# Optimization experiments

Measured on AMD Instinct MI355X. Metric: run time of the kernel, lower is better.

Reference implementation:

```python
import jax, jax.numpy as jnp
import numpy as np

N_NODES = 100_000
N_EDGES = 1_600_000
N_GRAPHS = 512
NF = 64        # n_node_feats
H1 = 128       # hidden width
H2 = 64        # dim_node_emb
DIM_OUT = 1
STEPS = 4      # set2set processing steps


def _lin(x, W, b):
    # torch Linear convention: y = x @ W.T + b, W: [out, in]
    return x @ W.T + b


def _gelu(x):
    return jax.nn.gelu(x, approximate=False)  # torch.nn.GELU default (erf)


def _lstm_cell(x, h, c, Wih, Whh, bih, bhh):
    g = x @ Wih.T + bih + h @ Whh.T + bhh
    i, f, gg, o = jnp.split(g, 4, axis=-1)  # torch gate order: i, f, g, o
    i, f, o = jax.nn.sigmoid(i), jax.nn.sigmoid(f), jax.nn.sigmoid(o)
    gg = jnp.tanh(gg)
    c = f * c + i * gg
    h = o * jnp.tanh(c)
    return h, c


def setup_inputs() -> dict:
    key = jax.random.key(0)
    ks = jax.random.split(key, 24)
    p = lambda k, shp: jax.random.normal(k, shp, dtype=jnp.float32) * 0.05
    inp = {
        "x": jax.random.normal(ks[0], (N_NODES, NF), dtype=jnp.float32),
        "edge_index": jax.random.randint(ks[1], (2, N_EDGES), 0, N_NODES, dtype=jnp.int32),
        "batch": jnp.sort(jax.random.randint(ks[2], (N_NODES,), 0, N_GRAPHS, dtype=jnp.int32)),
        "nfc_W": p(ks[3], (H1, NF)), "nfc_b": p(ks[4], (H1,)),
        "gc1_W": p(ks[5], (H1, H1)), "gc1_b": p(ks[6], (H1,)),
        "gc2_W": p(ks[7], (H2, H1)), "gc2_b": p(ks[8], (H2,)),
        "lstm0_Wih": p(ks[9], (4 * H2, 2 * H2)), "lstm0_Whh": p(ks[10], (4 * H2, H2)),
        "lstm0_bih": p(ks[11], (4 * H2,)), "lstm0_bhh": p(ks[12], (4 * H2,)),
        "lstm1_Wih": p(ks[13], (4 * H2, H2)), "lstm1_Whh": p(ks[14], (4 * H2, H2)),
        "lstm1_bih": p(ks[15], (4 * H2,)), "lstm1_bhh": p(ks[16], (4 * H2,)),
        "fc1_W": p(ks[17], (32, 2 * H2)), "fc1_b": p(ks[18], (32,)),
        "fc2_W": p(ks[19], (DIM_OUT, 32)), "fc2_b": p(ks[20], (DIM_OUT,)),
    }
    return inp


def _forward(x, edge_index, batch, nfc_W, nfc_b, gc1_W, gc1_b, gc2_W, gc2_b,
             lstm0_Wih, lstm0_Whh, lstm0_bih, lstm0_bhh,
             lstm1_Wih, lstm1_Whh, lstm1_bih, lstm1_bhh,
             fc1_W, fc1_b, fc2_W, fc2_b):
    src, dst = edge_index[0], edge_index[1]

    def gin_conv(h, W, b):
        # PyG GINConv, eps=0: lin((1+eps)*x + sum_{j in N(i)} x_j)
        agg = jax.ops.segment_sum(h[src], dst, num_segments=N_NODES)
        return _lin(h + agg, W, b)

    h = _gelu(_lin(x, nfc_W, nfc_b))
    h = _gelu(gin_conv(h, gc1_W, gc1_b))
    h = _gelu(gin_conv(h, gc2_W, gc2_b))
    # F.normalize(p=2, dim=1)
    h = h / jnp.maximum(jnp.linalg.norm(h, axis=1, keepdims=True), 1e-12)

    # Set2Set: 2-layer LSTM, 4 processing steps, scatter-softmax attention
    B = N_GRAPHS
    h0 = jnp.zeros((B, H2), jnp.float32); c0 = jnp.zeros((B, H2), jnp.float32)
    h1 = jnp.zeros((B, H2), jnp.float32); c1 = jnp.zeros((B, H2), jnp.float32)
    q_star = jnp.zeros((B, 2 * H2), jnp.float32)
    for _ in range(STEPS):
        h0, c0 = _lstm_cell(q_star, h0, c0, lstm0_Wih, lstm0_Whh, lstm0_bih, lstm0_bhh)
        h1, c1 = _lstm_cell(h0, h1, c1, lstm1_Wih, lstm1_Whh, lstm1_bih, lstm1_bhh)
        q = h1  # [B, H2]
        e = jnp.sum(h * q[batch], axis=-1, keepdims=True)  # [N, 1]
        m = jax.ops.segment_max(e, batch, num_segments=B)
        ex = jnp.exp(e - m[batch])
        s = jax.ops.segment_sum(ex, batch, num_segments=B)
        a = ex / (s[batch] + 1e-16)
        r = jax.ops.segment_sum(a * h, batch, num_segments=B)  # [B, H2]
        q_star = jnp.concatenate([q, r], axis=-1)

    z = _gelu(_lin(q_star, fc1_W, fc1_b))
    z = _lin(z, fc2_W, fc2_b)
    return z, h


def reference(x, edge_index, batch, nfc_W, nfc_b, gc1_W, gc1_b, gc2_W, gc2_b,
              lstm0_Wih, lstm0_Whh, lstm0_bih, lstm0_bhh,
              lstm1_Wih, lstm1_Whh, lstm1_bih, lstm1_bhh,
              fc1_W, fc1_b, fc2_W, fc2_b):
    return _forward(x, edge_index, batch, nfc_W, nfc_b, gc1_W, gc1_b, gc2_W, gc2_b,
                    lstm0_Wih, lstm0_Whh, lstm0_bih, lstm0_bhh,
                    lstm1_Wih, lstm1_Whh, lstm1_bih, lstm1_bhh,
                    fc1_W, fc1_b, fc2_W, fc2_b)
```

## Files before the change

kernel.cpp:

```cpp
#include <hip/hip_runtime.h>
#include <hip/hip_bf16.h>
#include <hip/hip_fp16.h>
#include <math.h>

constexpr int N  = 100000;
constexpr int E  = 1600000;
constexpr int NG = 512;
constexpr int NF = 64;
constexpr int H1 = 128;
constexpr int H2 = 64;

constexpr int BW   = 128;
constexpr int NB   = (N + BW - 1) / BW;
constexpr int CAP  = 2600;
constexpr int CHUNK = 4096;

constexpr int MAXN = 416;
constexpr int RST  = 68;

typedef __attribute__((ext_vector_type(8))) short short8;
typedef __attribute__((ext_vector_type(4))) float f32x4;

__device__ __forceinline__ float gelu_f(float x) {
    return 0.5f * x * (1.0f + erff(x * 0.70710678118654752f));
}
__device__ __forceinline__ float sigmoid_f(float x) {
    return 1.0f / (1.0f + expf(-x));
}
__device__ __forceinline__ float waveAllSum(float v) {
    #pragma unroll
    for (int m = 32; m; m >>= 1) v += __shfl_xor(v, m);
    return v;
}
__device__ __forceinline__ unsigned short f2bf(float x) {
    __hip_bfloat16 b = __float2bfloat16(x);
    return *reinterpret_cast<unsigned short*>(&b);
}
__device__ __forceinline__ float bf2f(unsigned short u) {
    return __uint_as_float(((unsigned int)u) << 16);
}
__device__ __forceinline__ float bf_lo(unsigned int u) { return __uint_as_float(u << 16); }
__device__ __forceinline__ float bf_hi(unsigned int u) { return __uint_as_float(u & 0xffff0000u); }

__device__ __forceinline__ void bfsplit(float v, unsigned short& hi, unsigned short& lo) {
    hi = f2bf(v);
    lo = f2bf(v - bf2f(hi));
}

__device__ __forceinline__ void pack8(float4 a, float4 b, short8& h8, short8& l8) {
    unsigned short h0,h1,h2,h3,h4,h5,h6,h7,l0,l1,l2,l3,l4,l5,l6,l7;
    bfsplit(a.x,h0,l0); bfsplit(a.y,h1,l1); bfsplit(a.z,h2,l2); bfsplit(a.w,h3,l3);
    bfsplit(b.x,h4,l4); bfsplit(b.y,h5,l5); bfsplit(b.z,h6,l6); bfsplit(b.w,h7,l7);
    union { uint4 u; short8 s; } th, tl;
    th.u = make_uint4((unsigned)h0|((unsigned)h1<<16),(unsigned)h2|((unsigned)h3<<16),
                      (unsigned)h4|((unsigned)h5<<16),(unsigned)h6|((unsigned)h7<<16));
    tl.u = make_uint4((unsigned)l0|((unsigned)l1<<16),(unsigned)l2|((unsigned)l3<<16),
                      (unsigned)l4|((unsigned)l5<<16),(unsigned)l6|((unsigned)l7<<16));
    h8 = th.s; l8 = tl.s;
}

__global__ __launch_bounds__(256) void setup_kernel(const int* __restrict__ batch,
                                                    const float* __restrict__ Wih0, const float* __restrict__ Whh0,
                                                    const float* __restrict__ bih0, const float* __restrict__ bhh0,
                                                    const float* __restrict__ Wih1, const float* __restrict__ Whh1,
                                                    const float* __restrict__ bih1, const float* __restrict__ bhh1,
                                                    const float* __restrict__ gc1W, const float* __restrict__ gc2W,
                                                    const float* __restrict__ nfcW,
                                                    float* __restrict__ WT0, float* __restrict__ WT1,
                                                    float* __restrict__ b0, float* __restrict__ b1,
                                                    unsigned short* __restrict__ W1F, unsigned short* __restrict__ W2F,
                                                    unsigned short* __restrict__ W0F,
                                                    int* __restrict__ bcursor, int* __restrict__ gstart) {
    int i = blockIdx.x * 256 + threadIdx.x;
    if (i < 192 * 256) {
        int k = i >> 8, j = i & 255;
        WT0[i] = (k < 128) ? Wih0[j * 128 + k] : Whh0[j * 64 + (k - 128)];
    }
    if (i < 128 * 256) {
        int k = i >> 8, j = i & 255;
        WT1[i] = (k < 64) ? Wih1[j * 64 + k] : Whh1[j * 64 + (k - 64)];
    }
    if (i < 16384) {
        int f = i >> 9, r = i & 511, l = r >> 3, j = r & 7;
        int c = f >> 3, ct = f & 7;
        int o = ct * 16 + (l & 15), k = c * 32 + (l >> 4) * 8 + j;
        unsigned short hi, lo;
        bfsplit(gc1W[o * 128 + k], hi, lo);
        W1F[f * 1024 + r] = hi;
        W1F[f * 1024 + 512 + r] = lo;
    }
    if (i < 8192) {
        int f = i >> 9, r = i & 511, l = r >> 3, j = r & 7;
        int c2 = f >> 2, ct2 = f & 3;
        int o = ct2 * 16 + (l & 15), k = c2 * 32 + (l >> 4) * 8 + j;
        unsigned short hi, lo;
        bfsplit(gc2W[o * 128 + k], hi, lo);
        W2F[f * 1024 + r] = hi;
        W2F[f * 1024 + 512 + r] = lo;
    }
    if (i < 8192) {
        int f = i >> 9, r = i & 511, l = r >> 3, j = r & 7;
        int c = f >> 3, ct = f & 7;
        int o = ct * 16 + (l & 15), k = c * 32 + (l >> 4) * 8 + j;
        unsigned short hi, lo;
        bfsplit(nfcW[o * 64 + k], hi, lo);
        W0F[f * 1024 + r] = hi;
        W0F[f * 1024 + 512 + r] = lo;
    }
    if (i < 256) { b0[i] = bih0[i] + bhh0[i]; b1[i] = bih1[i] + bhh1[i]; }
    if (i < NB) bcursor[i] = i * CAP;
    if (i <= NG) {
        if (i == NG) gstart[NG] = N;
        else {
            int lo = 0, hi = N;
            while (lo < hi) {
                int mid = (lo + hi) >> 1;
                if (batch[mid] < i) lo = mid + 1; else hi = mid;
            }
            gstart[i] = lo;
        }
    }
}

__global__ __launch_bounds__(256) void bin_scatter_kernel(const int* __restrict__ ei,
                                                          int* __restrict__ bcursor,
                                                          int* __restrict__ pairs) {
    __shared__ int hist[NB];
    __shared__ int start_s[NB];
    __shared__ int lcur[NB];
    int tid = threadIdx.x;
    int e0 = blockIdx.x * CHUNK;
    for (int b = tid; b < NB; b += 256) hist[b] = 0;
    __syncthreads();
    #pragma unroll 4
    for (int k = 0; k < CHUNK / 256; ++k) {
        int e = e0 + k * 256 + tid;
        if (e < E) atomicAdd(&hist[ei[E + e] >> 7], 1);
    }
    __syncthreads();
    for (int b = tid; b < NB; b += 256) {
        if (hist[b]) start_s[b] = atomicAdd(&bcursor[b], hist[b]);
        lcur[b] = 0;
    }
    __syncthreads();
    #pragma unroll 4
    for (int k = 0; k < CHUNK / 256; ++k) {
        int e = e0 + k * 256 + tid;
        if (e < E) {
            int d = ei[E + e];
            int s = ei[e];
            int b = d >> 7;
            int pos = start_s[b] + atomicAdd(&lcur[b], 1);
            if (pos < (b + 1) * CAP) pairs[pos] = (s << 7) | (d & 127);
        }
    }
}

__global__ __launch_bounds__(256) void csr_bucket_kernel(const int* __restrict__ pairs,
                                                         const int* __restrict__ bcursor,
                                                         int* __restrict__ srcs,
                                                         int2* __restrict__ nrange) {
    __shared__ int cnt_l[BW];
    __shared__ int cur_l[BW];
    __shared__ int wt[2];
    int b = blockIdx.x;
    int tid = threadIdx.x;
    int base = b * CAP;
    int cnt = bcursor[b] - base;
    if (cnt > CAP) cnt = CAP;
    if (tid < BW) cnt_l[tid] = 0;
    __syncthreads();
    for (int i = tid; i < cnt; i += 256) {
        atomicAdd(&cnt_l[pairs[base + i] & 127], 1);
    }
    __syncthreads();
    if (tid < BW) {
        int v = cnt_l[tid];
        int lane = tid & 63, w = tid >> 6;
        int incl = v;
        #pragma unroll
        for (int off = 1; off < 64; off <<= 1) {
            int t = __shfl_up(incl, off);
            if (lane >= off) incl += t;
        }
        if (lane == 63) wt[w] = incl;
        __syncthreads();
        int excl = (w ? wt[0] : 0) + incl - v;
        int node = b * BW + tid;
        if (node < N) nrange[node] = make_int2(base + excl, base + excl + v);
        cur_l[tid] = excl;
    } else {
        __syncthreads();
    }
    __syncthreads();
    for (int i = tid; i < cnt; i += 256) {
        int p = pairs[base + i];
        int pos = atomicAdd(&cur_l[p & 127], 1);
        srcs[base + pos] = p >> 7;
    }
}

__global__ __launch_bounds__(512, 2) void lin1_kernel(const float* __restrict__ x,
                                                      const uint4* __restrict__ W0F,
                                                      const float* __restrict__ bias,
                                                      unsigned short* __restrict__ out_bf, int nrows) {
    constexpr int EPS = 136;
    __shared__ __align__(16) uint4 w0lds[2048];
    __shared__ __align__(16) unsigned short eps[8][16 * EPS];
    union U8 { uint4 u; short8 s; };
    int tid = threadIdx.x, w = tid >> 6, lane = tid & 63;
    int m15 = lane & 15, quad = lane >> 4;
    int rowbase = blockIdx.x * 128 + w * 16;
    int r0 = rowbase + m15; if (r0 >= nrows) r0 = nrows - 1;

    #pragma unroll
    for (int i = 0; i < 4; ++i) w0lds[i * 512 + tid] = W0F[i * 512 + tid];
    __syncthreads();

    f32x4 acc[8];
    #pragma unroll
    for (int ct = 0; ct < 8; ++ct) acc[ct] = (f32x4)0.f;

    float4 p0[2][2];
    #pragma unroll
    for (int c = 0; c < 2; ++c) {
        p0[c][0] = *(const float4*)&x[(size_t)r0 * 64 + c * 32 + quad * 8];
        p0[c][1] = *(const float4*)&x[(size_t)r0 * 64 + c * 32 + quad * 8 + 4];
    }

    #pragma unroll
    for (int c = 0; c < 2; ++c) {
        short8 ah0, al0;
        pack8(p0[c][0], p0[c][1], ah0, al0);
        #pragma unroll
        for (int ct = 0; ct < 8; ++ct) {
            U8 th, tl;
            th.u = w0lds[(c * 8 + ct) * 128 + lane];
            tl.u = w0lds[(c * 8 + ct) * 128 + 64 + lane];
            short8 bh = th.s, bl = tl.s;
            acc[ct] = __builtin_amdgcn_mfma_f32_16x16x32_bf16(ah0, bh, acc[ct], 0, 0, 0);
            acc[ct] = __builtin_amdgcn_mfma_f32_16x16x32_bf16(ah0, bl, acc[ct], 0, 0, 0);
            acc[ct] = __builtin_amdgcn_mfma_f32_16x16x32_bf16(al0, bh, acc[ct], 0, 0, 0);
        }
    }

    unsigned short* ep = eps[w];
    #pragma unroll
    for (int ct = 0; ct < 8; ++ct) {
        float bc = bias[ct * 16 + m15];
        #pragma unroll
        for (int r = 0; r < 4; ++r) {
            int node = quad * 4 + r;
            ep[node * EPS + ct * 16 + m15] = f2bf(gelu_f(acc[ct][r] + bc));
        }
    }
    asm volatile("s_waitcnt lgkmcnt(0)" ::: "memory");
    #pragma unroll
    for (int it = 0; it < 4; ++it) {
        int idx = it * 64 + lane;
        int rowl = idx >> 4, off = (idx & 15) * 8;
        int grow = rowbase + rowl;
        if (grow < nrows)
            *(uint4*)(out_bf + (size_t)grow * 128 + off) = *(const uint4*)&ep[rowl * EPS + off];
    }
}

__global__ __launch_bounds__(256) void agg_half_kernel(const uint4* __restrict__ h4,
                                                       const int2* __restrict__ nrange,
                                                       const int* __restrict__ srcs,
                                                       uint4* __restrict__ utab,
                                                       int half) {
    int wave = threadIdx.x >> 6, lane = threadIdx.x & 63;
    int ew = lane >> 3, el = lane & 7;
    int n = blockIdx.x * 4 + wave;
    if (n >= N) return;
    int2 rng = nrange[n];
    int s0 = rng.x, deg = rng.y - rng.x;
    int m1 = deg < 64 ? deg : 64;
    int pre = (lane < m1) ? srcs[s0 + lane] : 0;
    int hofs = half * 8 + el;
    float a0 = 0.f, a1 = 0.f, a2 = 0.f, a3 = 0.f, a4 = 0.f, a5 = 0.f, a6 = 0.f, a7 = 0.f;
    auto addu = [&](uint4 u) {
        a0 += bf_lo(u.x); a1 += bf_hi(u.x); a2 += bf_lo(u.y); a3 += bf_hi(u.y);
        a4 += bf_lo(u.z); a5 += bf_hi(u.z); a6 += bf_lo(u.w); a7 += bf_hi(u.w);
    };
    int t = 0;
    for (; t + 16 <= m1; t += 16) {
        int i0 = __shfl(pre, t + ew);
        int i1 = __shfl(pre, t + 8 + ew);
        uint4 u0 = h4[(size_t)i0 * 16 + hofs];
        uint4 u1 = h4[(size_t)i1 * 16 + hofs];
        addu(u0); addu(u1);
    }
    for (; t < m1; t += 8) {
        int idx = t + ew;
        int s = __shfl(pre, idx < m1 ? idx : 0);
        if (idx < m1) addu(h4[(size_t)s * 16 + hofs]);
    }
    for (int j = 64 + ew; j < deg; j += 8) addu(h4[(size_t)srcs[s0 + j] * 16 + hofs]);
    a0 += __shfl_down(a0, 32); a1 += __shfl_down(a1, 32);
    a2 += __shfl_down(a2, 32); a3 += __shfl_down(a3, 32);
    a4 += __shfl_down(a4, 32); a5 += __shfl_down(a5, 32);
    a6 += __shfl_down(a6, 32); a7 += __shfl_down(a7, 32);
    a0 += __shfl_down(a0, 16); a1 += __shfl_down(a1, 16);
    a2 += __shfl_down(a2, 16); a3 += __shfl_down(a3, 16);
    a4 += __shfl_down(a4, 16); a5 += __shfl_down(a5, 16);
    a6 += __shfl_down(a6, 16); a7 += __shfl_down(a7, 16);
    a0 += __shfl_down(a0, 8);  a1 += __shfl_down(a1, 8);
    a2 += __shfl_down(a2, 8);  a3 += __shfl_down(a3, 8);
    a4 += __shfl_down(a4, 8);  a5 += __shfl_down(a5, 8);
    a6 += __shfl_down(a6, 8);  a7 += __shfl_down(a7, 8);
    if (ew == 0) {
        addu(h4[(size_t)n * 16 + hofs]);
        unsigned short h0, h1, h2, h3, h4_, h5, h6, h7;
        unsigned short l0, l1, l2, l3, l4, l5, l6, l7;
        bfsplit(a0, h0, l0); bfsplit(a1, h1, l1);
        bfsplit(a2, h2, l2); bfsplit(a3, h3, l3);
        bfsplit(a4, h4_, l4); bfsplit(a5, h5, l5);
        bfsplit(a6, h6, l6); bfsplit(a7, h7, l7);
        uint4 o0, o1;
        o0.x = (unsigned)h0 | ((unsigned)h1 << 16);
        o0.y = (unsigned)h2 | ((unsigned)h3 << 16);
        o0.z = (unsigned)l0 | ((unsigned)l1 << 16);
        o0.w = (unsigned)l2 | ((unsigned)l3 << 16);
        o1.x = (unsigned)h4_ | ((unsigned)h5 << 16);
        o1.y = (unsigned)h6 | ((unsigned)h7 << 16);
        o1.z = (unsigned)l4 | ((unsigned)l5 << 16);
        o1.w = (unsigned)l6 | ((unsigned)l7 << 16);
        int g0 = half * 16 + 2 * el;
        utab[(size_t)n * 32 + g0]     = o0;
        utab[(size_t)n * 32 + g0 + 1] = o1;
    }
}

__global__ __launch_bounds__(512, 2) void lin2_fused_kernel(const uint4* __restrict__ in4,
                                                            const uint4* __restrict__ W1F,
                                                            const float* __restrict__ b1,
                                                            const uint4* __restrict__ W2F,
                                                            unsigned short* __restrict__ y2,
                                                            int nrows) {
    constexpr int AST2 = 40;
    __shared__ __align__(16) uint4 wlds[6144];
    __shared__ __align__(16) unsigned short relds[8 * 1280];
    union U8 { uint4 u; short8 s; };
    int tid = threadIdx.x, w = tid >> 6, lane = tid & 63;
    int m15 = lane & 15, quad = lane >> 4;
    unsigned short* myL = relds + w * 1280;
    int rowbase = blockIdx.x * 128 + w * 16;
    int r0 = rowbase + m15; if (r0 >= nrows) r0 = nrows - 1;
    const uint4* a0p = in4 + (size_t)r0 * 32 + quad * 2;

    #pragma unroll
    for (int i = 0; i < 12; ++i) {
        int idx = i * 512 + tid;
        wlds[idx] = (idx < 4096) ? W1F[idx] : W2F[idx - 4096];
    }

    uint4 a[8];
    #pragma unroll
    for (int c = 0; c < 4; ++c) { a[2 * c] = a0p[c * 8]; a[2 * c + 1] = a0p[c * 8 + 1]; }

    float bc[8];
    #pragma unroll
    for (int ct = 0; ct < 8; ++ct) bc[ct] = b1[ct * 16 + m15];

    __syncthreads();
    const uint4* W1L = wlds;
    const uint4* W2L = wlds + 4096;

    f32x4 acc[8];
    #pragma unroll
    for (int ct = 0; ct < 8; ++ct) acc[ct] = (f32x4)0.f;

    #pragma unroll
    for (int c = 0; c < 4; ++c) {
        U8 t;
        uint4 u00 = a[2 * c], u01 = a[2 * c + 1];
        t.u = make_uint4(u00.x, u00.y, u01.x, u01.y); short8 ah0 = t.s;
        t.u = make_uint4(u00.z, u00.w, u01.z, u01.w); short8 al0 = t.s;
        #pragma unroll
        for (int ct = 0; ct < 8; ++ct) {
            U8 th, tl;
            th.u = W1L[(c * 8 + ct) * 128 + lane];
            tl.u = W1L[(c * 8 + ct) * 128 + 64 + lane];
            short8 bh = th.s, bl = tl.s;
            acc[ct] = __builtin_amdgcn_mfma_f32_16x16x32_bf16(ah0, bh, acc[ct], 0, 0, 0);
            acc[ct] = __builtin_amdgcn_mfma_f32_16x16x32_bf16(ah0, bl, acc[ct], 0, 0, 0);
            acc[ct] = __builtin_amdgcn_mfma_f32_16x16x32_bf16(al0, bh, acc[ct], 0, 0, 0);
        }
    }

    #pragma unroll
    for (int ct = 0; ct < 8; ++ct)
        #pragma unroll
        for (int r = 0; r < 4; ++r)
            acc[ct][r] = gelu_f(acc[ct][r] + bc[ct]);

    unsigned short* Ahi2 = myL;
    unsigned short* Alo2 = myL + 16 * AST2;
    f32x4 acc2[4];
    #pragma unroll
    for (int ct = 0; ct < 4; ++ct) acc2[ct] = (f32x4)0.f;

    #pragma unroll
    for (int c2 = 0; c2 < 4; ++c2) {
        #pragma unroll
        for (int cc = 0; cc < 2; ++cc) {
            int ct = c2 * 2 + cc;
            #pragma unroll
            for (int r = 0; r < 4; ++r) {
                int node = quad * 4 + r;
                unsigned short hi, lo;
                bfsplit(acc[ct][r], hi, lo);
                Ahi2[node * AST2 + cc * 16 + m15] = hi;
                Alo2[node * AST2 + cc * 16 + m15] = lo;
            }
        }
        asm volatile("s_waitcnt lgkmcnt(0)" ::: "memory");
        short8 ah0 = *(const short8*)&Ahi2[m15 * AST2 + quad * 8];
        short8 al0 = *(const short8*)&Alo2[m15 * AST2 + quad * 8];
        #pragma unroll
        for (int ct2 = 0; ct2 < 4; ++ct2) {
            U8 th, tl;
            th.u = W2L[(c2 * 4 + ct2) * 128 + lane];
            tl.u = W2L[(c2 * 4 + ct2) * 128 + 64 + lane];
            short8 bh = th.s, bl = tl.s;
            acc2[ct2] = __builtin_amdgcn_mfma_f32_16x16x32_bf16(ah0, bh, acc2[ct2], 0, 0, 0);
            acc2[ct2] = __builtin_amdgcn_mfma_f32_16x16x32_bf16(ah0, bl, acc2[ct2], 0, 0, 0);
            acc2[ct2] = __builtin_amdgcn_mfma_f32_16x16x32_bf16(al0, bh, acc2[ct2], 0, 0, 0);
        }
    }

    unsigned short* ep = myL;
    #pragma unroll
    for (int ct2 = 0; ct2 < 4; ++ct2)
        #pragma unroll
        for (int r = 0; r < 4; ++r) {
            int node = quad * 4 + r;
            __half hv = __float2half(acc2[ct2][r]);
            ep[node * 72 + ct2 * 16 + m15] = *reinterpret_cast<unsigned short*>(&hv);
        }
    asm volatile("s_waitcnt lgkmcnt(0)" ::: "memory");
    #pragma unroll
    for (int it = 0; it < 2; ++it) {
        int idx = it * 64 + lane;
        int rowl = idx >> 3, off = (idx & 7) * 8;
        int grow = rowbase + rowl;
        if (grow < nrows)
            *(uint4*)(y2 + (size_t)grow * 64 + off) = *(const uint4*)&ep[rowl * 72 + off];
    }
}

__global__ __launch_bounds__(256) void agg2_norm_kernel(const uint2* __restrict__ y2,
                                                        const int2* __restrict__ nrange,
                                                        const int* __restrict__ srcs,
                                                        const float* __restrict__ b2,
                                                        float* __restrict__ hn) {
    int wave = threadIdx.x >> 6, lane = threadIdx.x & 63;
    int qw = lane >> 4, ql = lane & 15;
    int n = blockIdx.x * 4 + wave;
    if (n >= N) return;
    int2 rng = nrange[n];
    int s0 = rng.x, deg = rng.y - rng.x;
    int m1 = deg < 64 ? deg : 64;
    int pre = (lane < m1) ? srcs[s0 + lane] : 0;
    float a0 = 0.f, a1 = 0.f, a2 = 0.f, a3 = 0.f;
    auto addu = [&](uint2 u) {
        float2 f01 = __half22float2(*reinterpret_cast<__half2*>(&u.x));
        float2 f23 = __half22float2(*reinterpret_cast<__half2*>(&u.y));
        a0 += f01.x; a1 += f01.y; a2 += f23.x; a3 += f23.y;
    };
    int t = 0;
    for (; t + 16 <= m1; t += 16) {
        int i0 = __shfl(pre, t + qw);
        int i1 = __shfl(pre, t + 4 + qw);
        int i2 = __shfl(pre, t + 8 + qw);
        int i3 = __shfl(pre, t + 12 + qw);
        uint2 u0 = y2[(size_t)i0 * 16 + ql];
        uint2 u1 = y2[(size_t)i1 * 16 + ql];
        uint2 u2 = y2[(size_t)i2 * 16 + ql];
        uint2 u3 = y2[(size_t)i3 * 16 + ql];
        addu(u0); addu(u1); addu(u2); addu(u3);
    }
    for (; t < m1; t += 4) {
        int idx = t + qw;
        int s = __shfl(pre, idx < m1 ? idx : 0);
        if (idx < m1) addu(y2[(size_t)s * 16 + ql]);
    }
    for (int j = 64 + qw; j < deg; j += 4) addu(y2[(size_t)srcs[s0 + j] * 16 + ql]);
    a0 += __shfl_down(a0, 32); a1 += __shfl_down(a1, 32);
    a2 += __shfl_down(a2, 32); a3 += __shfl_down(a3, 32);
    a0 += __shfl_down(a0, 16); a1 += __shfl_down(a1, 16);
    a2 += __shfl_down(a2, 16); a3 += __shfl_down(a3, 16);
    if (qw == 0) {
        addu(y2[(size_t)n * 16 + ql]);
        float4 bv = *(const float4*)&b2[ql * 4];
        float v0 = gelu_f(a0 + bv.x), v1 = gelu_f(a1 + bv.y);
        float v2 = gelu_f(a2 + bv.z), v3 = gelu_f(a3 + bv.w);
        float ss = v0 * v0 + v1 * v1 + v2 * v2 + v3 * v3;
        #pragma unroll
        for (int mm = 1; mm < 16; mm <<= 1) ss += __shfl_xor(ss, mm);
        float d = fmaxf(sqrtf(ss), 1e-12f);
        *(float4*)&hn[(size_t)n * 64 + ql * 4] = make_float4(v0 / d, v1 / d, v2 / d, v3 / d);
    }
}

__global__ __launch_bounds__(256) void set2set_kernel(const float* __restrict__ hn,
                                                      const int* __restrict__ gstart,
                                                      const float* __restrict__ WT0, const float* __restrict__ b0,
                                                      const float* __restrict__ WT1, const float* __restrict__ b1,
                                                      const float* __restrict__ fc1W, const float* __restrict__ fc1b,
                                                      const float* __restrict__ fc2W, const float* __restrict__ fc2b,
                                                      float* __restrict__ zout) {
    __shared__ __align__(16) unsigned short hL[MAXN * RST];
    __shared__ float av[MAXN];
    __shared__ __align__(16) float xc0[192];
    __shared__ __align__(16) float xc1[128];
    __shared__ __align__(16) float gates[256];
    __shared__ float c0v[H2], c1v[H2];
    __shared__ float red[4];
    __shared__ float rp[4][H2];
    __shared__ float sp[4];
    __shared__ float fcWT[128 * 32];

    int g = blockIdx.x;
    int tid = threadIdx.x, w = tid >> 6, lane = tid & 63;
    int s0 = gstart[g], s1 = gstart[g + 1];
    int cnt = s1 - s0;
    int cL = cnt < MAXN ? cnt : MAXN;
    const float* hq = xc1 + 64;

    for (int idx = tid; idx < cL * 16; idx += 256) {
        int n = idx >> 4, p4 = idx & 15;
        float4 v = *(const float4*)&hn[(size_t)(s0 + n) * 64 + p4 * 4];
        uint2 u;
        u.x = (unsigned int)f2bf(v.x) | ((unsigned int)f2bf(v.y) << 16);
        u.y = (unsigned int)f2bf(v.z) | ((unsigned int)f2bf(v.w) << 16);
        *(uint2*)&hL[n * RST + p4 * 4] = u;
    }
    for (int i = tid; i < 4096; i += 256) {
        int j = i >> 7, k = i & 127;
        fcWT[k * 32 + j] = fc1W[i];
    }
    if (tid < 192) xc0[tid] = 0.f;
    if (tid < 128) xc1[tid] = 0.f;
    if (tid < H2) { c0v[tid] = 0.f; c1v[tid] = 0.f; }
    float b0v = b0[tid], b1v = b1[tid];
    __syncthreads();

    for (int step = 0; step < 4; ++step) {
        {
            float a0 = 0.f, a1 = 0.f, a2 = 0.f, a3 = 0.f;
            #pragma unroll 8
            for (int k = 0; k < 192; k += 4) {
                a0 += xc0[k]     * WT0[(k)     * 256 + tid];
                a1 += xc0[k + 1] * WT0[(k + 1) * 256 + tid];
                a2 += xc0[k + 2] * WT0[(k + 2) * 256 + tid];
                a3 += xc0[k + 3] * WT0[(k + 3) * 256 + tid];
            }
            gates[tid] = (a0 + a1) + (a2 + a3) + b0v;
        }
        __syncthreads();
        if (tid < H2) {
            float ii = sigmoid_f(gates[tid]), ff = sigmoid_f(gates[H2 + tid]);
            float gg = tanhf(gates[2 * H2 + tid]), oo = sigmoid_f(gates[3 * H2 + tid]);
            float c = ff * c0v[tid] + ii * gg;
            float h = oo * tanhf(c);
            c0v[tid] = c; xc0[128 + tid] = h; xc1[tid] = h;
        }
        __syncthreads();
        {
            float a0 = 0.f, a1 = 0.f, a2 = 0.f, a3 = 0.f;
            #pragma unroll 8
            for (int k = 0; k < 128; k += 4) {
                a0 += xc1[k]     * WT1[(k)     * 256 + tid];
                a1 += xc1[k + 1] * WT1[(k + 1) * 256 + tid];
                a2 += xc1[k + 2] * WT1[(k + 2) * 256 + tid];
                a3 += xc1[k + 3] * WT1[(k + 3) * 256 + tid];
            }
            gates[tid] = (a0 + a1) + (a2 + a3) + b1v;
        }
        __syncthreads();
        if (tid < H2) {
            float ii = sigmoid_f(gates[tid]), ff = sigmoid_f(gates[H2 + tid]);
            float gg = tanhf(gates[2 * H2 + tid]), oo = sigmoid_f(gates[3 * H2 + tid]);
            float c = ff * c1v[tid] + ii * gg;
            float h = oo * tanhf(c);
            c1v[tid] = c; xc1[64 + tid] = h;
        }
        __syncthreads();

        float lm = -INFINITY;
        for (int i = tid; i < cnt; i += 256) {
            float e = 0.f;
            if (i < MAXN) {
                const uint2* row = (const uint2*)&hL[i * RST];
                #pragma unroll
                for (int p4 = 0; p4 < 16; ++p4) {
                    uint2 u = row[p4];
                    e += bf_lo(u.x) * hq[p4 * 4 + 0];
                    e += bf_hi(u.x) * hq[p4 * 4 + 1];
                    e += bf_lo(u.y) * hq[p4 * 4 + 2];
                    e += bf_hi(u.y) * hq[p4 * 4 + 3];
                }
                av[i] = e;
            } else {
                for (int f = 0; f < 64; ++f) e += hn[(size_t)(s0 + i) * 64 + f] * hq[f];
            }
            lm = fmaxf(lm, e);
        }
        #pragma unroll
        for (int mm = 32; mm; mm >>= 1) lm = fmaxf(lm, __shfl_xor(lm, mm));
        if (lane == 0) red[w] = lm;
        __syncthreads();
        float m = fmaxf(fmaxf(red[0], red[1]), fmaxf(red[2], red[3]));

        float ps = 0.f;
        for (int i = tid; i < cnt; i += 256) {
            float e;
            if (i < MAXN) e = av[i];
            else {
                e = 0.f;
                for (int f = 0; f < 64; ++f) e += hn[(size_t)(s0 + i) * 64 + f] * hq[f];
            }
            float p = expf(e - m);
            ps += p;
            if (i < MAXN) av[i] = p;
        }
        ps = waveAllSum(ps);
        if (lane == 0) sp[w] = ps;
        __syncthreads();
        float s = sp[0] + sp[1] + sp[2] + sp[3];

        float racc = 0.f;
        for (int i = w; i < cL; i += 4) {
            unsigned short hv = hL[i * RST + lane];
            racc += av[i] * bf2f(hv);
        }
        float qf = hq[lane];
        for (int n = MAXN + w; n < cnt; n += 4) {
            float v = hn[(size_t)(s0 + n) * 64 + lane];
            float e = waveAllSum(v * qf);
            float p = expf(e - m);
            racc += p * v;
        }
        rp[w][lane] = racc;
        __syncthreads();
        if (tid < H2) {
            float r = 0.f;
            if (cnt > 0) {
                r = (rp[0][tid] + rp[1][tid] + rp[2][tid] + rp[3][tid]) / (s + 1e-16f);
            }
            xc0[tid] = xc1[64 + tid];
            xc0[H2 + tid] = r;
        }
        __syncthreads();
    }

    if (w == 0) {
        float zv = 0.f;
        if (lane < 32) {
            float a = fc1b[lane];
            #pragma unroll 8
            for (int k = 0; k < 128; ++k) a += xc0[k] * fcWT[k * 32 + lane];
            zv = gelu_f(a) * fc2W[lane];
        }
        zv = waveAllSum(zv);
        if (lane == 0) zout[g] = zv + fc2b[0];
    }
}

extern "C" void kernel_launch(void* const* d_in, const int* in_sizes, int n_in,
                              void* d_out, int out_size, void* d_ws, size_t ws_size,
                              hipStream_t stream) {
    const float* x       = (const float*)d_in[0];
    const int*   ei      = (const int*)d_in[1];
    const int*   batch   = (const int*)d_in[2];
    const float* nfc_W   = (const float*)d_in[3];
    const float* nfc_b   = (const float*)d_in[4];
    const float* gc1_W   = (const float*)d_in[5];
    const float* gc1_b   = (const float*)d_in[6];
    const float* gc2_W   = (const float*)d_in[7];
    const float* gc2_b   = (const float*)d_in[8];
    const float* l0_Wih  = (const float*)d_in[9];
    const float* l0_Whh  = (const float*)d_in[10];
    const float* l0_bih  = (const float*)d_in[11];
    const float* l0_bhh  = (const float*)d_in[12];
    const float* l1_Wih  = (const float*)d_in[13];
    const float* l1_Whh  = (const float*)d_in[14];
    const float* l1_bih  = (const float*)d_in[15];
    const float* l1_bhh  = (const float*)d_in[16];
    const float* fc1_W   = (const float*)d_in[17];
    const float* fc1_b   = (const float*)d_in[18];
    const float* fc2_W   = (const float*)d_in[19];
    const float* fc2_b   = (const float*)d_in[20];

    float* out = (float*)d_out;
    float* hn_out = out + NG;

    char* p = (char*)d_ws;
    auto take = [&](size_t bytes) {
        char* r = p;
        p += (bytes + 255) & ~size_t(255);
        return r;
    };
    float*          sbuf  = (float*)take((size_t)N * H1 * 4);
    unsigned short* hbbuf = (unsigned short*)take((size_t)N * H1 * 2);
    int*   srcs   = (int*)take((size_t)NB * CAP * 4);
    int2*  nrange = (int2*)take((size_t)N * 8);
    int*   bcursor= (int*)take((size_t)NB * 4);
    int*   gstart = (int*)take((size_t)(NG + 1) * 4);
    float* WT0    = (float*)take((size_t)192 * 256 * 4);
    float* WT1    = (float*)take((size_t)128 * 256 * 4);
    float* b0     = (float*)take((size_t)256 * 4);
    float* b1     = (float*)take((size_t)256 * 4);
    unsigned short* W1F = (unsigned short*)take((size_t)32 * 1024 * 2);
    unsigned short* W2F = (unsigned short*)take((size_t)16 * 1024 * 2);
    unsigned short* W0F = (unsigned short*)take((size_t)16 * 1024 * 2);

    int* pairs = (int*)sbuf;

    setup_kernel<<<192, 256, 0, stream>>>(batch, l0_Wih, l0_Whh, l0_bih, l0_bhh,
                                          l1_Wih, l1_Whh, l1_bih, l1_bhh,
                                          gc1_W, gc2_W, nfc_W,
                                          WT0, WT1, b0, b1, W1F, W2F, W0F, bcursor, gstart);

    bin_scatter_kernel<<<(E + CHUNK - 1) / CHUNK, 256, 0, stream>>>(ei, bcursor, pairs);
    csr_bucket_kernel<<<NB, 256, 0, stream>>>(pairs, bcursor, srcs, nrange);

    int linGrid = (N + 127) / 128;
    lin1_kernel<<<linGrid, 512, 0, stream>>>(x, (const uint4*)W0F, nfc_b, hbbuf, N);
    agg_half_kernel<<<(N + 3) / 4, 256, 0, stream>>>((const uint4*)hbbuf, nrange, srcs,
                                                     (uint4*)sbuf, 0);
    agg_half_kernel<<<(N + 3) / 4, 256, 0, stream>>>((const uint4*)hbbuf, nrange, srcs,
                                                     (uint4*)sbuf, 1);
    lin2_fused_kernel<<<linGrid, 512, 0, stream>>>((const uint4*)sbuf, (const uint4*)W1F, gc1_b,
                                                   (const uint4*)W2F, hbbuf, N);
    agg2_norm_kernel<<<(N + 3) / 4, 256, 0, stream>>>((const uint2*)hbbuf, nrange, srcs,
                                                      gc2_b, hn_out);

    set2set_kernel<<<NG, 256, 0, stream>>>(hn_out, gstart, WT0, b0, WT1, b1,
                                           fc1_W, fc1_b, fc2_W, fc2_b, out);
}
```

Measured before the change: 423.1 us.

## Merge split-half layer-1 aggregation into one pass and widen layer-2 gather loads

The first GIN aggregation ran as two launches, each gathering one 128-byte half of every 256-byte bf16 row with 8 lanes per edge. It now runs as one kernel in which 16 lanes fetch the full row per edge, 4 edges per step, which removes a launch and the second read of the CSR index and neighbour list. The second aggregation moves from 8-byte fp16 loads with 16 lanes per 128-byte row to 16-byte loads with 8 lanes per row, 8 edges at a time, plus a 32-edge unrolled loop. The trade-off is less memory-level parallelism per edge in the first kernel's split, higher register use from the extra accumulators, and a deeper shuffle reduction in the second kernel.

```diff
diff --git a/kernel.cpp b/kernel.cpp
--- a/kernel.cpp
+++ b/kernel.cpp
@@ -265,20 +265,18 @@
     }
 }
 
-__global__ __launch_bounds__(256) void agg_half_kernel(const uint4* __restrict__ h4,
-                                                       const int2* __restrict__ nrange,
-                                                       const int* __restrict__ srcs,
-                                                       uint4* __restrict__ utab,
-                                                       int half) {
+__global__ __launch_bounds__(256) void agg_kernel(const uint4* __restrict__ h4,
+                                                  const int2* __restrict__ nrange,
+                                                  const int* __restrict__ srcs,
+                                                  uint4* __restrict__ utab) {
     int wave = threadIdx.x >> 6, lane = threadIdx.x & 63;
-    int ew = lane >> 3, el = lane & 7;
+    int qw = lane >> 4, ql = lane & 15;
     int n = blockIdx.x * 4 + wave;
     if (n >= N) return;
     int2 rng = nrange[n];
     int s0 = rng.x, deg = rng.y - rng.x;
     int m1 = deg < 64 ? deg : 64;
     int pre = (lane < m1) ? srcs[s0 + lane] : 0;
-    int hofs = half * 8 + el;
     float a0 = 0.f, a1 = 0.f, a2 = 0.f, a3 = 0.f, a4 = 0.f, a5 = 0.f, a6 = 0.f, a7 = 0.f;
     auto addu = [&](uint4 u) {
         a0 += bf_lo(u.x); a1 += bf_hi(u.x); a2 += bf_lo(u.y); a3 += bf_hi(u.y);
@@ -286,18 +284,22 @@
     };
     int t = 0;
     for (; t + 16 <= m1; t += 16) {
-        int i0 = __shfl(pre, t + ew);
-        int i1 = __shfl(pre, t + 8 + ew);
-        uint4 u0 = h4[(size_t)i0 * 16 + hofs];
-        uint4 u1 = h4[(size_t)i1 * 16 + hofs];
-        addu(u0); addu(u1);
-    }
-    for (; t < m1; t += 8) {
-        int idx = t + ew;
+        int i0 = __shfl(pre, t + qw);
+        int i1 = __shfl(pre, t + 4 + qw);
+        int i2 = __shfl(pre, t + 8 + qw);
+        int i3 = __shfl(pre, t + 12 + qw);
+        uint4 u0 = h4[(size_t)i0 * 16 + ql];
+        uint4 u1 = h4[(size_t)i1 * 16 + ql];
+        uint4 u2 = h4[(size_t)i2 * 16 + ql];
+        uint4 u3 = h4[(size_t)i3 * 16 + ql];
+        addu(u0); addu(u1); addu(u2); addu(u3);
+    }
+    for (; t < m1; t += 4) {
+        int idx = t + qw;
         int s = __shfl(pre, idx < m1 ? idx : 0);
-        if (idx < m1) addu(h4[(size_t)s * 16 + hofs]);
-    }
-    for (int j = 64 + ew; j < deg; j += 8) addu(h4[(size_t)srcs[s0 + j] * 16 + hofs]);
+        if (idx < m1) addu(h4[(size_t)s * 16 + ql]);
+    }
+    for (int j = 64 + qw; j < deg; j += 4) addu(h4[(size_t)srcs[s0 + j] * 16 + ql]);
     a0 += __shfl_down(a0, 32); a1 += __shfl_down(a1, 32);
     a2 += __shfl_down(a2, 32); a3 += __shfl_down(a3, 32);
     a4 += __shfl_down(a4, 32); a5 += __shfl_down(a5, 32);
@@ -306,12 +308,8 @@
     a2 += __shfl_down(a2, 16); a3 += __shfl_down(a3, 16);
     a4 += __shfl_down(a4, 16); a5 += __shfl_down(a5, 16);
     a6 += __shfl_down(a6, 16); a7 += __shfl_down(a7, 16);
-    a0 += __shfl_down(a0, 8);  a1 += __shfl_down(a1, 8);
-    a2 += __shfl_down(a2, 8);  a3 += __shfl_down(a3, 8);
-    a4 += __shfl_down(a4, 8);  a5 += __shfl_down(a5, 8);
-    a6 += __shfl_down(a6, 8);  a7 += __shfl_down(a7, 8);
-    if (ew == 0) {
-        addu(h4[(size_t)n * 16 + hofs]);
+    if (qw == 0) {
+        addu(h4[(size_t)n * 16 + ql]);
         unsigned short h0, h1, h2, h3, h4_, h5, h6, h7;
         unsigned short l0, l1, l2, l3, l4, l5, l6, l7;
         bfsplit(a0, h0, l0); bfsplit(a1, h1, l1);
@@ -327,9 +325,8 @@
         o1.y = (unsigned)h6 | ((unsigned)h7 << 16);
         o1.z = (unsigned)l4 | ((unsigned)l5 << 16);
         o1.w = (unsigned)l6 | ((unsigned)l7 << 16);
-        int g0 = half * 16 + 2 * el;
-        utab[(size_t)n * 32 + g0]     = o0;
-        utab[(size_t)n * 32 + g0 + 1] = o1;
+        utab[(size_t)n * 32 + 2 * ql]     = o0;
+        utab[(size_t)n * 32 + 2 * ql + 1] = o1;
     }
 }
 
@@ -451,57 +448,80 @@
     }
 }
 
-__global__ __launch_bounds__(256) void agg2_norm_kernel(const uint2* __restrict__ y2,
+__global__ __launch_bounds__(256) void agg2_norm_kernel(const uint4* __restrict__ y4,
                                                         const int2* __restrict__ nrange,
                                                         const int* __restrict__ srcs,
                                                         const float* __restrict__ b2,
                                                         float* __restrict__ hn) {
     int wave = threadIdx.x >> 6, lane = threadIdx.x & 63;
-    int qw = lane >> 4, ql = lane & 15;
+    int ew = lane >> 3, el = lane & 7;
     int n = blockIdx.x * 4 + wave;
     if (n >= N) return;
     int2 rng = nrange[n];
     int s0 = rng.x, deg = rng.y - rng.x;
     int m1 = deg < 64 ? deg : 64;
     int pre = (lane < m1) ? srcs[s0 + lane] : 0;
-    float a0 = 0.f, a1 = 0.f, a2 = 0.f, a3 = 0.f;
-    auto addu = [&](uint2 u) {
+    float a0 = 0.f, a1 = 0.f, a2 = 0.f, a3 = 0.f, a4 = 0.f, a5 = 0.f, a6 = 0.f, a7 = 0.f;
+    auto addu = [&](uint4 u) {
         float2 f01 = __half22float2(*reinterpret_cast<__half2*>(&u.x));
         float2 f23 = __half22float2(*reinterpret_cast<__half2*>(&u.y));
+        float2 f45 = __half22float2(*reinterpret_cast<__half2*>(&u.z));
+        float2 f67 = __half22float2(*reinterpret_cast<__half2*>(&u.w));
         a0 += f01.x; a1 += f01.y; a2 += f23.x; a3 += f23.y;
+        a4 += f45.x; a5 += f45.y; a6 += f67.x; a7 += f67.y;
     };
     int t = 0;
+    for (; t + 32 <= m1; t += 32) {
+        int i0 = __shfl(pre, t + ew);
+        int i1 = __shfl(pre, t + 8 + ew);
+        int i2 = __shfl(pre, t + 16 + ew);
+        int i3 = __shfl(pre, t + 24 + ew);
+        uint4 u0 = y4[(size_t)i0 * 8 + el];
+        uint4 u1 = y4[(size_t)i1 * 8 + el];
+        uint4 u2 = y4[(size_t)i2 * 8 + el];
+        uint4 u3 = y4[(size_t)i3 * 8 + el];
+        addu(u0); addu(u1); addu(u2); addu(u3);
+    }
     for (; t + 16 <= m1; t += 16) {
-        int i0 = __shfl(pre, t + qw);
-        int i1 = __shfl(pre, t + 4 + qw);
-        int i2 = __shfl(pre, t + 8 + qw);
-        int i3 = __shfl(pre, t + 12 + qw);
-        uint2 u0 = y2[(size_t)i0 * 16 + ql];
-        uint2 u1 = y2[(size_t)i1 * 16 + ql];
-        uint2 u2 = y2[(size_t)i2 * 16 + ql];
-        uint2 u3 = y2[(size_t)i3 * 16 + ql];
-        addu(u0); addu(u1); addu(u2); addu(u3);
-    }
-    for (; t < m1; t += 4) {
-        int idx = t + qw;
+        int i0 = __shfl(pre, t + ew);
+        int i1 = __shfl(pre, t + 8 + ew);
+        uint4 u0 = y4[(size_t)i0 * 8 + el];
+        uint4 u1 = y4[(size_t)i1 * 8 + el];
+        addu(u0); addu(u1);
+    }
+    for (; t < m1; t += 8) {
+        int idx = t + ew;
         int s = __shfl(pre, idx < m1 ? idx : 0);
-        if (idx < m1) addu(y2[(size_t)s * 16 + ql]);
-    }
-    for (int j = 64 + qw; j < deg; j += 4) addu(y2[(size_t)srcs[s0 + j] * 16 + ql]);
+        if (idx < m1) addu(y4[(size_t)s * 8 + el]);
+    }
+    for (int j = 64 + ew; j < deg; j += 8) addu(y4[(size_t)srcs[s0 + j] * 8 + el]);
     a0 += __shfl_down(a0, 32); a1 += __shfl_down(a1, 32);
     a2 += __shfl_down(a2, 32); a3 += __shfl_down(a3, 32);
+    a4 += __shfl_down(a4, 32); a5 += __shfl_down(a5, 32);
+    a6 += __shfl_down(a6, 32); a7 += __shfl_down(a7, 32);
     a0 += __shfl_down(a0, 16); a1 += __shfl_down(a1, 16);
     a2 += __shfl_down(a2, 16); a3 += __shfl_down(a3, 16);
-    if (qw == 0) {
-        addu(y2[(size_t)n * 16 + ql]);
-        float4 bv = *(const float4*)&b2[ql * 4];
-        float v0 = gelu_f(a0 + bv.x), v1 = gelu_f(a1 + bv.y);
-        float v2 = gelu_f(a2 + bv.z), v3 = gelu_f(a3 + bv.w);
-        float ss = v0 * v0 + v1 * v1 + v2 * v2 + v3 * v3;
-        #pragma unroll
-        for (int mm = 1; mm < 16; mm <<= 1) ss += __shfl_xor(ss, mm);
+    a4 += __shfl_down(a4, 16); a5 += __shfl_down(a5, 16);
+    a6 += __shfl_down(a6, 16); a7 += __shfl_down(a7, 16);
+    a0 += __shfl_down(a0, 8);  a1 += __shfl_down(a1, 8);
+    a2 += __shfl_down(a2, 8);  a3 += __shfl_down(a3, 8);
+    a4 += __shfl_down(a4, 8);  a5 += __shfl_down(a5, 8);
+    a6 += __shfl_down(a6, 8);  a7 += __shfl_down(a7, 8);
+    if (ew == 0) {
+        addu(y4[(size_t)n * 8 + el]);
+        float4 bv0 = *(const float4*)&b2[el * 8];
+        float4 bv1 = *(const float4*)&b2[el * 8 + 4];
+        float v0 = gelu_f(a0 + bv0.x), v1 = gelu_f(a1 + bv0.y);
+        float v2 = gelu_f(a2 + bv0.z), v3 = gelu_f(a3 + bv0.w);
+        float v4 = gelu_f(a4 + bv1.x), v5 = gelu_f(a5 + bv1.y);
+        float v6 = gelu_f(a6 + bv1.z), v7 = gelu_f(a7 + bv1.w);
+        float ss = v0 * v0 + v1 * v1 + v2 * v2 + v3 * v3
+                 + v4 * v4 + v5 * v5 + v6 * v6 + v7 * v7;
+        #pragma unroll
+        for (int mm = 1; mm < 8; mm <<= 1) ss += __shfl_xor(ss, mm);
         float d = fmaxf(sqrtf(ss), 1e-12f);
-        *(float4*)&hn[(size_t)n * 64 + ql * 4] = make_float4(v0 / d, v1 / d, v2 / d, v3 / d);
+        *(float4*)&hn[(size_t)n * 64 + el * 8]     = make_float4(v0 / d, v1 / d, v2 / d, v3 / d);
+        *(float4*)&hn[(size_t)n * 64 + el * 8 + 4] = make_float4(v4 / d, v5 / d, v6 / d, v7 / d);
     }
 }
 
@@ -730,13 +750,10 @@
 
     int linGrid = (N + 127) / 128;
     lin1_kernel<<<linGrid, 512, 0, stream>>>(x, (const uint4*)W0F, nfc_b, hbbuf, N);
-    agg_half_kernel<<<(N + 3) / 4, 256, 0, stream>>>((const uint4*)hbbuf, nrange, srcs,
-                                                     (uint4*)sbuf, 0);
-    agg_half_kernel<<<(N + 3) / 4, 256, 0, stream>>>((const uint4*)hbbuf, nrange, srcs,
-                                                     (uint4*)sbuf, 1);
+    agg_kernel<<<(N + 3) / 4, 256, 0, stream>>>((const uint4*)hbbuf, nrange, srcs, (uint4*)sbuf);
     lin2_fused_kernel<<<linGrid, 512, 0, stream>>>((const uint4*)sbuf, (const uint4*)W1F, gc1_b,
                                                    (const uint4*)W2F, hbbuf, N);
-    agg2_norm_kernel<<<(N + 3) / 4, 256, 0, stream>>>((const uint2*)hbbuf, nrange, srcs,
+    agg2_norm_kernel<<<(N + 3) / 4, 256, 0, stream>>>((const uint4*)hbbuf, nrange, srcs,
                                                       gc2_b, hn_out);
 
     set2set_kernel<<<NG, 256, 0, stream>>>(hn_out, gstart, WT0, b0, WT1, b1,
```

After: 414.1 us. -2.1%, faster.
